# Kernel tuning notes

Measured on AMD Instinct MI355X. Metric: run time of the kernel, lower is better.

## Reference

```python
import jax, jax.numpy as jnp
import numpy as np

N_NODES = 50000
N_EDGES = 800000
D = 128
N_GRAPHS = 64
N_CLASSES = 10


def setup_inputs() -> dict:
    key = jax.random.key(0)
    ks = jax.random.split(key, 10)
    x = jax.random.normal(ks[0], (N_NODES, D), dtype=jnp.float32)
    edge_index = jax.random.randint(ks[1], (2, N_EDGES), 0, N_NODES, dtype=jnp.int64)
    batch = jnp.sort(jax.random.randint(ks[2], (N_NODES,), 0, N_GRAPHS, dtype=jnp.int64))
    s = 1.0 / np.sqrt(D)
    W1a = jax.random.uniform(ks[3], (D, D), jnp.float32, -s, s)
    W1b = jax.random.uniform(ks[4], (D, D), jnp.float32, -s, s)
    W2a = jax.random.uniform(ks[5], (D, D), jnp.float32, -s, s)
    W2b = jax.random.uniform(ks[6], (D, D), jnp.float32, -s, s)
    Wfc = jax.random.uniform(ks[7], (D, N_CLASSES), jnp.float32, -s, s)
    return {
        "x": x, "edge_index": edge_index, "batch": batch,
        "W1a": W1a, "b1a": jnp.zeros((D,), jnp.float32),
        "W1b": W1b, "b1b": jnp.zeros((D,), jnp.float32),
        "W2a": W2a, "b2a": jnp.zeros((D,), jnp.float32),
        "W2b": W2b, "b2b": jnp.zeros((D,), jnp.float32),
        "Wfc": Wfc, "bfc": jnp.zeros((N_CLASSES,), jnp.float32),
    }


def _gin_conv(x, src, dst, Wa, ba, Wb, bb):
    # sum aggregation of neighbor messages x[src] into dst (eps = 0)
    agg = jax.ops.segment_sum(x[src], dst, num_segments=N_NODES)
    h = x + agg  # (1 + eps) * x + sum_{j->i} x_j
    h = jax.nn.relu(h @ Wa + ba)
    h = jax.nn.relu(h @ Wb + bb)
    return h


def reference(x, edge_index, batch, W1a, b1a, W1b, b1b, W2a, b2a, W2b, b2b, Wfc, bfc):
    src, dst = edge_index[0], edge_index[1]
    h = _gin_conv(x, src, dst, W1a, b1a, W1b, b1b)
    h = _gin_conv(h, src, dst, W2a, b2a, W2b, b2b)
    # global mean pool over graphs
    sums = jax.ops.segment_sum(h, batch, num_segments=N_GRAPHS)
    counts = jax.ops.segment_sum(jnp.ones((h.shape[0], 1), h.dtype), batch, num_segments=N_GRAPHS)
    pooled = sums / jnp.maximum(counts, 1.0)
    logits = pooled @ Wfc + bfc
    return jax.nn.sigmoid(logits)
```

## Files before the change

### kernel.cpp

```cpp
#include <hip/hip_runtime.h>

#define NN 50000
#define NE 800000
#define DF 128
#define NG 64
#define NC 10
#define NBK 98
#define PART_CHUNK 4096
#define PART_GRID 196
#define ACAP 12288
#define FINE_CAP 12288
#define RT 136

typedef short bf16x8 __attribute__((ext_vector_type(8)));
typedef float f32x4  __attribute__((ext_vector_type(4)));

__device__ __forceinline__ void atomAddF(float* p, float v) {
  __hip_atomic_fetch_add(p, v, __ATOMIC_RELAXED, __HIP_MEMORY_SCOPE_AGENT);
}
__device__ __forceinline__ float b2f(unsigned short u) {
  union { unsigned int i; float f; } v; v.i = (unsigned int)u << 16; return v.f;
}
__device__ __forceinline__ unsigned int f2b(float f) {
  unsigned int i = __float_as_uint(f);
  return (i + 0x7fffu + ((i >> 16) & 1u)) >> 16;
}

__global__ __launch_bounds__(256) void k_cast(const float* __restrict__ x,
                                              unsigned short* __restrict__ xb)
{
  const int i = blockIdx.x * 256 + threadIdx.x;
  if (i * 4 >= NN * DF) return;
  const float4 v = reinterpret_cast<const float4*>(x)[i];
  uint2 o;
  o.x = f2b(v.x) | (f2b(v.y) << 16);
  o.y = f2b(v.z) | (f2b(v.w) << 16);
  reinterpret_cast<uint2*>(xb)[i] = o;
}

__global__ __launch_bounds__(256) void k_prepw(const float* __restrict__ W0,
                                               const float* __restrict__ W1,
                                               const float* __restrict__ W2,
                                               const float* __restrict__ W3,
                                               unsigned short* __restrict__ Wt)
{
  const int o = blockIdx.x * 256 + threadIdx.x;
  if (o >= 4 * 2048) return;
  const int mat = o >> 11;
  const float* W = (mat == 0) ? W0 : (mat == 1) ? W1 : (mat == 2) ? W2 : W3;
  const int rem = o & 2047;
  const int n  = rem >> 4;
  const int k0 = (rem & 15) * 8;
  unsigned int u[8];
#pragma unroll
  for (int j = 0; j < 8; ++j) u[j] = f2b(W[(size_t)(k0 + j) * DF + n]);
  uint4 p;
  p.x = u[0] | (u[1] << 16);
  p.y = u[2] | (u[3] << 16);
  p.z = u[4] | (u[5] << 16);
  p.w = u[6] | (u[7] << 16);
  *reinterpret_cast<uint4*>(Wt + (size_t)mat * DF * DF + (size_t)n * DF + k0) = p;
}

__global__ __launch_bounds__(256) void k_part(const int* __restrict__ src,
                                              const int* __restrict__ dst,
                                              int* __restrict__ cnt_b,
                                              unsigned int* __restrict__ arena)
{
  __shared__ unsigned int stage[PART_CHUNK];
  __shared__ int lhist[128], lcnt[128], lcur[128], gbase[128];
  const int tid = threadIdx.x;
  const int e0  = blockIdx.x * PART_CHUNK;
  const int nE  = min(PART_CHUNK, NE - e0);

  for (int i = tid; i < 128; i += 256) lhist[i] = 0;
  __syncthreads();

  unsigned int pk[16];
  int bk[16];
#pragma unroll
  for (int i = 0; i < 16; ++i) {
    const int e = e0 + i * 256 + tid;
    if (e < NE) {
      const int d = dst[e];
      const int s = src[e];
      const int b = d >> 9;
      bk[i] = b;
      pk[i] = ((unsigned int)b << 25) | ((unsigned int)(d & 511) << 16) | (unsigned int)s;
      atomicAdd(&lhist[b], 1);
    } else {
      bk[i] = -1;
    }
  }
  __syncthreads();
  for (int i = tid; i < 128; i += 256) lcnt[i] = lhist[i];
  __syncthreads();
  for (int off = 1; off < 128; off <<= 1) {
    int v = 0;
    if (tid < 128 && tid >= off) v = lhist[tid - off];
    __syncthreads();
    if (tid < 128) lhist[tid] += v;
    __syncthreads();
  }
  if (tid < 128) lcur[tid] = lhist[tid] - lcnt[tid];
  __syncthreads();
#pragma unroll
  for (int i = 0; i < 16; ++i) {
    if (bk[i] >= 0) {
      const int pos = atomicAdd(&lcur[bk[i]], 1);
      stage[pos] = pk[i];
    }
  }
  __syncthreads();
  if (tid < NBK) {
    const int c = lcnt[tid];
    if (c > 0) gbase[tid] = atomicAdd(&cnt_b[tid], c);
  }
  __syncthreads();
  for (int idx = tid; idx < nE; idx += 256) {
    const unsigned int p = stage[idx];
    const int b = (int)(p >> 25);
    const int loff = lhist[b] - lcnt[b];
    arena[(size_t)b * ACAP + gbase[b] + (idx - loff)] = p;
  }
}

__global__ __launch_bounds__(128) void k_bscan(const int* __restrict__ cnt_b,
                                               int* __restrict__ base_b,
                                               int* __restrict__ rs)
{
  __shared__ int sm[128];
  const int t = threadIdx.x;
  const int v = (t < NBK) ? cnt_b[t] : 0;
  sm[t] = v;
  __syncthreads();
  for (int off = 1; off < 128; off <<= 1) {
    int u = (t >= off) ? sm[t - off] : 0;
    __syncthreads();
    sm[t] += u;
    __syncthreads();
  }
  base_b[t] = sm[t] - v;
  if (t == NBK - 1) rs[NN] = sm[t];
}

__global__ __launch_bounds__(256) void k_fine(const unsigned int* __restrict__ arena,
                                              const int* __restrict__ cnt_b,
                                              const int* __restrict__ base_b,
                                              int* __restrict__ rs,
                                              unsigned short* __restrict__ es)
{
  __shared__ unsigned short les[FINE_CAP];
  __shared__ int bins[4096];
  __shared__ int partials[256];
  const int tid   = threadIdx.x;
  const int b     = blockIdx.x;
  const int cnt   = cnt_b[b];
  const int wbase = base_b[b];
  const int nbase = b << 9;
  const int nwin  = min(512, NN - nbase);
  const unsigned int* ap = arena + (size_t)b * ACAP;

  for (int i = tid; i < 4096; i += 256) bins[i] = 0;
  __syncthreads();
  for (int idx = tid; idx < cnt; idx += 256) {
    const unsigned int p = ap[idx];
    const int key = (int)(((p >> 16) & 511) << 3) | (int)((p & 0xffffu) >> 13);
    atomicAdd(&bins[key], 1);
  }
  __syncthreads();
  const int b16 = tid * 16;
  int sum = 0;
#pragma unroll
  for (int k = 0; k < 16; ++k) sum += bins[b16 + k];
  partials[tid] = sum;
  __syncthreads();
  for (int off = 1; off < 256; off <<= 1) {
    int u = (tid >= off) ? partials[tid - off] : 0;
    __syncthreads();
    partials[tid] += u;
    __syncthreads();
  }
  int run = partials[tid] - sum;
#pragma unroll
  for (int k = 0; k < 16; ++k) {
    const int v = bins[b16 + k];
    bins[b16 + k] = run;
    run += v;
  }
  __syncthreads();
  for (int i = tid; i < nwin; i += 256) rs[nbase + i] = wbase + bins[i << 3];
  __syncthreads();
  if (cnt <= FINE_CAP) {
    for (int idx = tid; idx < cnt; idx += 256) {
      const unsigned int p = ap[idx];
      const int key = (int)(((p >> 16) & 511) << 3) | (int)((p & 0xffffu) >> 13);
      const int pos = atomicAdd(&bins[key], 1);
      les[pos] = (unsigned short)(p & 0xffffu);
    }
    __syncthreads();
    for (int i = tid; i < cnt; i += 256) es[wbase + i] = les[i];
  } else {
    for (int idx = tid; idx < cnt; idx += 256) {
      const unsigned int p = ap[idx];
      const int key = (int)(((p >> 16) & 511) << 3) | (int)((p & 0xffffu) >> 13);
      const int pos = atomicAdd(&bins[key], 1);
      es[wbase + pos] = (unsigned short)(p & 0xffffu);
    }
  }
}

__global__ __launch_bounds__(256) void k_gather(const unsigned short* __restrict__ feat,
                                                unsigned short* __restrict__ outp,
                                                const int* __restrict__ rs,
                                                const unsigned short* __restrict__ es)
{
  const int wid  = (blockIdx.x * 256 + threadIdx.x) >> 6;
  const int lane = threadIdx.x & 63;
  if (wid >= NN) return;
  const int beg = rs[wid];
  const int end = rs[wid + 1];
  const int off = lane * 2;

  const unsigned int self = *reinterpret_cast<const unsigned int*>(feat + (size_t)wid * DF + off);
  float ax = b2f(self & 0xffff), ay = b2f(self >> 16);
  int j = beg;
  while (j < end && (j & 3)) {
    const int s = es[j];
    const unsigned int u = *reinterpret_cast<const unsigned int*>(feat + (size_t)s * DF + off);
    ax += b2f(u & 0xffff);
    ay += b2f(u >> 16);
    ++j;
  }
  for (; j + 3 < end; j += 4) {
    const uint2 e4 = *reinterpret_cast<const uint2*>(es + j);
    const int s0 = (int)(e4.x & 0xffffu), s1 = (int)(e4.x >> 16);
    const int s2 = (int)(e4.y & 0xffffu), s3 = (int)(e4.y >> 16);
    const unsigned int u0 = *reinterpret_cast<const unsigned int*>(feat + (size_t)s0 * DF + off);
    const unsigned int u1 = *reinterpret_cast<const unsigned int*>(feat + (size_t)s1 * DF + off);
    const unsigned int u2 = *reinterpret_cast<const unsigned int*>(feat + (size_t)s2 * DF + off);
    const unsigned int u3 = *reinterpret_cast<const unsigned int*>(feat + (size_t)s3 * DF + off);
    ax += b2f(u0 & 0xffff) + b2f(u1 & 0xffff) + b2f(u2 & 0xffff) + b2f(u3 & 0xffff);
    ay += b2f(u0 >> 16)    + b2f(u1 >> 16)    + b2f(u2 >> 16)    + b2f(u3 >> 16);
  }
  for (; j < end; ++j) {
    const int s = es[j];
    const unsigned int u = *reinterpret_cast<const unsigned int*>(feat + (size_t)s * DF + off);
    ax += b2f(u & 0xffff);
    ay += b2f(u >> 16);
  }
  const unsigned int o = f2b(ax) | (f2b(ay) << 16);
  *reinterpret_cast<unsigned int*>(outp + (size_t)wid * DF + off) = o;
}

__global__ __launch_bounds__(256) void k_gemm2(const unsigned short* __restrict__ Ab,
                                               const unsigned short* __restrict__ Wta,
                                               const float* __restrict__ ba,
                                               const unsigned short* __restrict__ Wtb,
                                               const float* __restrict__ bb,
                                               unsigned short* __restrict__ outb, int M)
{
  __shared__ unsigned short WbL[128 * 128];
  __shared__ unsigned short hL[4][16 * RT];
  const int tid  = threadIdx.x;
  const int lane = tid & 63;
  const int w    = tid >> 6;
  const int col  = lane & 15;
  const int kq   = lane >> 4;

  for (int i = tid; i < 2048; i += 256) {
    const int n = i >> 4, kb = i & 15;
    const int kbp = (kb + n) & 15;
    *reinterpret_cast<uint4*>(&WbL[n * 128 + kbp * 8]) =
        *reinterpret_cast<const uint4*>(&Wtb[(size_t)n * 128 + kb * 8]);
  }

  bf16x8 wfa[8][4];
#pragma unroll
  for (int nf = 0; nf < 8; ++nf)
#pragma unroll
    for (int s = 0; s < 4; ++s)
      wfa[nf][s] = *reinterpret_cast<const bf16x8*>(
          Wta + (size_t)(nf * 16 + col) * DF + s * 32 + kq * 8);

  __syncthreads();

  unsigned short* hw = &hL[w][0];
  const int rbase = blockIdx.x * 256;

  int m = rbase + w * 16 + col;
  int mld = (m < M) ? m : (M - 1);
  bf16x8 bc[4];
#pragma unroll
  for (int s = 0; s < 4; ++s)
    bc[s] = *reinterpret_cast<const bf16x8*>(Ab + (size_t)mld * DF + s * 32 + kq * 8);

#pragma unroll
  for (int t = 0; t < 4; ++t) {
    bf16x8 bn[4];
    if (t < 3) {
      const int m2 = rbase + (t + 1) * 64 + w * 16 + col;
      const int mld2 = (m2 < M) ? m2 : (M - 1);
#pragma unroll
      for (int s = 0; s < 4; ++s)
        bn[s] = *reinterpret_cast<const bf16x8*>(Ab + (size_t)mld2 * DF + s * 32 + kq * 8);
    }
    f32x4 acc[8];
#pragma unroll
    for (int nf = 0; nf < 8; ++nf) acc[nf] = (f32x4){0.f, 0.f, 0.f, 0.f};
#pragma unroll
    for (int s = 0; s < 4; ++s)
#pragma unroll
      for (int nf = 0; nf < 8; ++nf)
        acc[nf] = __builtin_amdgcn_mfma_f32_16x16x32_bf16(wfa[nf][s], bc[s], acc[nf], 0, 0, 0);
#pragma unroll
    for (int nf = 0; nf < 8; ++nf) {
      const float4 bv = *reinterpret_cast<const float4*>(ba + nf * 16 + kq * 4);
      uint2 pk;
      pk.x = f2b(fmaxf(acc[nf][0] + bv.x, 0.f)) | (f2b(fmaxf(acc[nf][1] + bv.y, 0.f)) << 16);
      pk.y = f2b(fmaxf(acc[nf][2] + bv.z, 0.f)) | (f2b(fmaxf(acc[nf][3] + bv.w, 0.f)) << 16);
      *reinterpret_cast<uint2*>(&hw[col * RT + nf * 16 + kq * 4]) = pk;
    }
    asm volatile("s_waitcnt lgkmcnt(0)" ::: "memory");
    __builtin_amdgcn_sched_barrier(0);
    f32x4 acc2[8];
#pragma unroll
    for (int nf = 0; nf < 8; ++nf) acc2[nf] = (f32x4){0.f, 0.f, 0.f, 0.f};
#pragma unroll
    for (int s = 0; s < 4; ++s) {
      const bf16x8 hb = *reinterpret_cast<const bf16x8*>(&hw[col * RT + s * 32 + kq * 8]);
#pragma unroll
      for (int nf = 0; nf < 8; ++nf) {
        const int kbp = (s * 4 + kq + col) & 15;
        const bf16x8 wb = *reinterpret_cast<const bf16x8*>(&WbL[(nf * 16 + col) * 128 + kbp * 8]);
        acc2[nf] = __builtin_amdgcn_mfma_f32_16x16x32_bf16(wb, hb, acc2[nf], 0, 0, 0);
      }
    }
    if (m < M) {
#pragma unroll
      for (int nf = 0; nf < 8; ++nf) {
        const float4 bv = *reinterpret_cast<const float4*>(bb + nf * 16 + kq * 4);
        ushort4 p;
        p.x = (unsigned short)f2b(fmaxf(acc2[nf][0] + bv.x, 0.f));
        p.y = (unsigned short)f2b(fmaxf(acc2[nf][1] + bv.y, 0.f));
        p.z = (unsigned short)f2b(fmaxf(acc2[nf][2] + bv.z, 0.f));
        p.w = (unsigned short)f2b(fmaxf(acc2[nf][3] + bv.w, 0.f));
        *reinterpret_cast<ushort4*>(outb + (size_t)m * DF + nf * 16 + kq * 4) = p;
      }
    }
#pragma unroll
    for (int s = 0; s < 4; ++s) bc[s] = bn[s];
    m = rbase + (t + 1) * 64 + w * 16 + col;
    mld = (m < M) ? m : (M - 1);
  }
}

__global__ __launch_bounds__(256) void k_pool(const unsigned short* __restrict__ h,
                                              const int* __restrict__ batch,
                                              float* __restrict__ sums,
                                              int* __restrict__ cnts)
{
  const int wv   = (blockIdx.x * 256 + threadIdx.x) >> 6;
  const int lane = threadIdx.x & 63;
  const int n0 = wv * 32;
  if (n0 >= NN) return;
  const int n1 = min(n0 + 32, NN);
  const int off = lane * 2;

  const int gfirst = batch[n0];
  const int glast  = batch[n1 - 1];
  float ax = 0.f, ay = 0.f;

  if (gfirst == glast) {
#pragma unroll 4
    for (int i = n0; i < n1; ++i) {
      const unsigned int u = *reinterpret_cast<const unsigned int*>(h + (size_t)i * DF + off);
      ax += b2f(u & 0xffff);
      ay += b2f(u >> 16);
    }
    atomAddF(&sums[gfirst * DF + off],     ax);
    atomAddF(&sums[gfirst * DF + off + 1], ay);
    if (lane == 0) atomicAdd(&cnts[gfirst], n1 - n0);
  } else {
    int g = gfirst, cnt = 0;
    for (int i = n0; i < n1; ++i) {
      const int gi = batch[i];
      if (gi != g) {
        atomAddF(&sums[g * DF + off],     ax);
        atomAddF(&sums[g * DF + off + 1], ay);
        if (lane == 0) atomicAdd(&cnts[g], cnt);
        ax = 0.f; ay = 0.f; cnt = 0; g = gi;
      }
      const unsigned int u = *reinterpret_cast<const unsigned int*>(h + (size_t)i * DF + off);
      ax += b2f(u & 0xffff);
      ay += b2f(u >> 16);
      ++cnt;
    }
    atomAddF(&sums[g * DF + off],     ax);
    atomAddF(&sums[g * DF + off + 1], ay);
    if (lane == 0) atomicAdd(&cnts[g], cnt);
  }
}

__global__ __launch_bounds__(256) void k_head(const float* __restrict__ sums,
                                              const int* __restrict__ cnts,
                                              const float* __restrict__ Wfc,
                                              const float* __restrict__ bfc,
                                              float* __restrict__ out)
{
  for (int o = threadIdx.x; o < NG * NC; o += 256) {
    const int g = o / NC, c = o % NC;
    const float inv = 1.f / fmaxf((float)cnts[g], 1.f);
    float z = bfc[c];
    for (int k = 0; k < DF; ++k)
      z = fmaf(sums[g * DF + k] * inv, Wfc[k * NC + c], z);
    out[o] = 1.f / (1.f + expf(-z));
  }
}

extern "C" void kernel_launch(void* const* d_in, const int* in_sizes, int n_in,
                              void* d_out, int out_size, void* d_ws, size_t ws_size,
                              hipStream_t stream)
{
  const float* x   = (const float*)d_in[0];
  const int*   ei  = (const int*)d_in[1];
  const int* batch = (const int*)d_in[2];
  const float* W1a = (const float*)d_in[3];
  const float* b1a = (const float*)d_in[4];
  const float* W1b = (const float*)d_in[5];
  const float* b1b = (const float*)d_in[6];
  const float* W2a = (const float*)d_in[7];
  const float* b2a = (const float*)d_in[8];
  const float* W2b = (const float*)d_in[9];
  const float* b2b = (const float*)d_in[10];
  const float* Wfc = (const float*)d_in[11];
  const float* bfc = (const float*)d_in[12];
  float* out = (float*)d_out;

  const int* src = ei;
  const int* dst = ei + NE;

  unsigned short* xb = (unsigned short*)d_ws;
  unsigned short* A  = xb + (size_t)NN * DF;
  unsigned short* H  = A + (size_t)NN * DF;
  unsigned short* Wt = H + (size_t)NN * DF;
  float* sums  = (float*)(Wt + (size_t)4 * DF * DF);
  int*   cnts  = (int*)(sums + NG * DF);
  int*   cnt_b = cnts + 64;
  int*   base_b= cnt_b + 128;
  int*   rs    = base_b + 128;
  unsigned short* es = (unsigned short*)(rs + (NN + 4));
  unsigned int* arena = (unsigned int*)(es + NE);

  unsigned short* Wt1a = Wt;
  unsigned short* Wt1b = Wt + DF * DF;
  unsigned short* Wt2a = Wt + 2 * DF * DF;
  unsigned short* Wt2b = Wt + 3 * DF * DF;

  const int gemm_grid   = (NN + 255) / 256;
  const int gather_grid = (NN * 64 + 255) / 256;
  const int pool_grid   = ((NN + 31) / 32 + 3) / 4;

  k_cast<<<(NN * DF / 4 + 255) / 256, 256, 0, stream>>>(x, xb);
  k_prepw<<<32, 256, 0, stream>>>(W1a, W1b, W2a, W2b, Wt);
  hipMemsetAsync(sums, 0, (size_t)(NG * DF + 64 + 128) * sizeof(float), stream);
  k_part<<<PART_GRID, 256, 0, stream>>>(src, dst, cnt_b, arena);
  k_bscan<<<1, 128, 0, stream>>>(cnt_b, base_b, rs);
  k_fine<<<NBK, 256, 0, stream>>>(arena, cnt_b, base_b, rs, es);

  k_gather<<<gather_grid, 256, 0, stream>>>(xb, A, rs, es);
  k_gemm2<<<gemm_grid, 256, 0, stream>>>(A, Wt1a, b1a, Wt1b, b1b, A, NN);

  k_gather<<<gather_grid, 256, 0, stream>>>(A, H, rs, es);
  k_gemm2<<<gemm_grid, 256, 0, stream>>>(H, Wt2a, b2a, Wt2b, b2b, H, NN);

  k_pool<<<pool_grid, 256, 0, stream>>>(H, batch, sums, cnts);
  k_head<<<1, 256, 0, stream>>>(sums, cnts, Wfc, bfc, out);
}
```

Baseline: 205.0 us.

## Reblock weights k-major and run fused MLP GEMM with 512-thread blocks

Changes the prepared weight layout so each (k-block, n) 8-element chunk is contiguous, which lets the second weight matrix be copied linearly into LDS and read without the skewed bank-swizzle. The fused two-layer GEMM now uses 512-thread blocks handling 128 rows each (one tile per wave) instead of 256-thread blocks that looped over 4 tiles with software prefetch. Biases are hoisted into registers. This trades the in-block prefetch pipelining and weight reuse across tiles for more parallelism and simpler code, and the new unswizzled LDS layout may bring bank conflicts.

New measurement: 191.6 us. 6.5% less time.

```diff
diff --git a/kernel.cpp b/kernel.cpp
--- a/kernel.cpp
+++ b/kernel.cpp
@@ -49,17 +49,17 @@
   const int mat = o >> 11;
   const float* W = (mat == 0) ? W0 : (mat == 1) ? W1 : (mat == 2) ? W2 : W3;
   const int rem = o & 2047;
-  const int n  = rem >> 4;
-  const int k0 = (rem & 15) * 8;
+  const int kb = rem >> 7;
+  const int n  = rem & 127;
   unsigned int u[8];
 #pragma unroll
-  for (int j = 0; j < 8; ++j) u[j] = f2b(W[(size_t)(k0 + j) * DF + n]);
+  for (int j = 0; j < 8; ++j) u[j] = f2b(W[(size_t)(kb * 8 + j) * DF + n]);
   uint4 p;
   p.x = u[0] | (u[1] << 16);
   p.y = u[2] | (u[3] << 16);
   p.z = u[4] | (u[5] << 16);
   p.w = u[6] | (u[7] << 16);
-  *reinterpret_cast<uint4*>(Wt + (size_t)mat * DF * DF + (size_t)n * DF + k0) = p;
+  *reinterpret_cast<uint4*>(Wt + (size_t)mat * DF * DF + (size_t)rem * 8) = p;
 }
 
 __global__ __launch_bounds__(256) void k_part(const int* __restrict__ src,
@@ -253,27 +253,24 @@
   *reinterpret_cast<unsigned int*>(outp + (size_t)wid * DF + off) = o;
 }
 
-__global__ __launch_bounds__(256) void k_gemm2(const unsigned short* __restrict__ Ab,
+__global__ __launch_bounds__(512) void k_gemm2(const unsigned short* __restrict__ Ab,
                                                const unsigned short* __restrict__ Wta,
                                                const float* __restrict__ ba,
                                                const unsigned short* __restrict__ Wtb,
                                                const float* __restrict__ bb,
                                                unsigned short* __restrict__ outb, int M)
 {
-  __shared__ unsigned short WbL[128 * 128];
-  __shared__ unsigned short hL[4][16 * RT];
+  __shared__ unsigned short WbL[2048 * 8];
+  __shared__ unsigned short hL[8][16 * RT];
   const int tid  = threadIdx.x;
   const int lane = tid & 63;
   const int w    = tid >> 6;
   const int col  = lane & 15;
   const int kq   = lane >> 4;
 
-  for (int i = tid; i < 2048; i += 256) {
-    const int n = i >> 4, kb = i & 15;
-    const int kbp = (kb + n) & 15;
-    *reinterpret_cast<uint4*>(&WbL[n * 128 + kbp * 8]) =
-        *reinterpret_cast<const uint4*>(&Wtb[(size_t)n * 128 + kb * 8]);
-  }
+  for (int i = tid; i < 2048; i += 512)
+    *reinterpret_cast<uint4*>(&WbL[i * 8]) =
+        *reinterpret_cast<const uint4*>(&Wtb[(size_t)i * 8]);
 
   bf16x8 wfa[8][4];
 #pragma unroll
@@ -281,77 +278,68 @@
 #pragma unroll
     for (int s = 0; s < 4; ++s)
       wfa[nf][s] = *reinterpret_cast<const bf16x8*>(
-          Wta + (size_t)(nf * 16 + col) * DF + s * 32 + kq * 8);
+          Wta + ((size_t)(s * 4 + kq) * 128 + nf * 16 + col) * 8);
+
+  float4 bva[8], bvb[8];
+#pragma unroll
+  for (int nf = 0; nf < 8; ++nf) {
+    bva[nf] = *reinterpret_cast<const float4*>(ba + nf * 16 + kq * 4);
+    bvb[nf] = *reinterpret_cast<const float4*>(bb + nf * 16 + kq * 4);
+  }
 
   __syncthreads();
 
   unsigned short* hw = &hL[w][0];
-  const int rbase = blockIdx.x * 256;
-
-  int m = rbase + w * 16 + col;
-  int mld = (m < M) ? m : (M - 1);
+  const int m   = blockIdx.x * 128 + w * 16 + col;
+  const int mld = (m < M) ? m : (M - 1);
+
   bf16x8 bc[4];
 #pragma unroll
   for (int s = 0; s < 4; ++s)
     bc[s] = *reinterpret_cast<const bf16x8*>(Ab + (size_t)mld * DF + s * 32 + kq * 8);
 
-#pragma unroll
-  for (int t = 0; t < 4; ++t) {
-    bf16x8 bn[4];
-    if (t < 3) {
-      const int m2 = rbase + (t + 1) * 64 + w * 16 + col;
-      const int mld2 = (m2 < M) ? m2 : (M - 1);
-#pragma unroll
-      for (int s = 0; s < 4; ++s)
-        bn[s] = *reinterpret_cast<const bf16x8*>(Ab + (size_t)mld2 * DF + s * 32 + kq * 8);
-    }
-    f32x4 acc[8];
-#pragma unroll
-    for (int nf = 0; nf < 8; ++nf) acc[nf] = (f32x4){0.f, 0.f, 0.f, 0.f};
-#pragma unroll
-    for (int s = 0; s < 4; ++s)
-#pragma unroll
-      for (int nf = 0; nf < 8; ++nf)
-        acc[nf] = __builtin_amdgcn_mfma_f32_16x16x32_bf16(wfa[nf][s], bc[s], acc[nf], 0, 0, 0);
+  f32x4 acc[8];
+#pragma unroll
+  for (int nf = 0; nf < 8; ++nf) acc[nf] = (f32x4){0.f, 0.f, 0.f, 0.f};
+#pragma unroll
+  for (int s = 0; s < 4; ++s)
+#pragma unroll
+    for (int nf = 0; nf < 8; ++nf)
+      acc[nf] = __builtin_amdgcn_mfma_f32_16x16x32_bf16(wfa[nf][s], bc[s], acc[nf], 0, 0, 0);
+
+#pragma unroll
+  for (int nf = 0; nf < 8; ++nf) {
+    uint2 pk;
+    pk.x = f2b(fmaxf(acc[nf][0] + bva[nf].x, 0.f)) | (f2b(fmaxf(acc[nf][1] + bva[nf].y, 0.f)) << 16);
+    pk.y = f2b(fmaxf(acc[nf][2] + bva[nf].z, 0.f)) | (f2b(fmaxf(acc[nf][3] + bva[nf].w, 0.f)) << 16);
+    *reinterpret_cast<uint2*>(&hw[col * RT + nf * 16 + kq * 4]) = pk;
+  }
+  asm volatile("s_waitcnt lgkmcnt(0)" ::: "memory");
+  __builtin_amdgcn_sched_barrier(0);
+
+  f32x4 acc2[8];
+#pragma unroll
+  for (int nf = 0; nf < 8; ++nf) acc2[nf] = (f32x4){0.f, 0.f, 0.f, 0.f};
+#pragma unroll
+  for (int s = 0; s < 4; ++s) {
+    const bf16x8 hb = *reinterpret_cast<const bf16x8*>(&hw[col * RT + s * 32 + kq * 8]);
 #pragma unroll
     for (int nf = 0; nf < 8; ++nf) {
-      const float4 bv = *reinterpret_cast<const float4*>(ba + nf * 16 + kq * 4);
-      uint2 pk;
-      pk.x = f2b(fmaxf(acc[nf][0] + bv.x, 0.f)) | (f2b(fmaxf(acc[nf][1] + bv.y, 0.f)) << 16);
-      pk.y = f2b(fmaxf(acc[nf][2] + bv.z, 0.f)) | (f2b(fmaxf(acc[nf][3] + bv.w, 0.f)) << 16);
-      *reinterpret_cast<uint2*>(&hw[col * RT + nf * 16 + kq * 4]) = pk;
-    }
-    asm volatile("s_waitcnt lgkmcnt(0)" ::: "memory");
-    __builtin_amdgcn_sched_barrier(0);
-    f32x4 acc2[8];
-#pragma unroll
-    for (int nf = 0; nf < 8; ++nf) acc2[nf] = (f32x4){0.f, 0.f, 0.f, 0.f};
-#pragma unroll
-    for (int s = 0; s < 4; ++s) {
-      const bf16x8 hb = *reinterpret_cast<const bf16x8*>(&hw[col * RT + s * 32 + kq * 8]);
-#pragma unroll
-      for (int nf = 0; nf < 8; ++nf) {
-        const int kbp = (s * 4 + kq + col) & 15;
-        const bf16x8 wb = *reinterpret_cast<const bf16x8*>(&WbL[(nf * 16 + col) * 128 + kbp * 8]);
-        acc2[nf] = __builtin_amdgcn_mfma_f32_16x16x32_bf16(wb, hb, acc2[nf], 0, 0, 0);
-      }
-    }
-    if (m < M) {
-#pragma unroll
-      for (int nf = 0; nf < 8; ++nf) {
-        const float4 bv = *reinterpret_cast<const float4*>(bb + nf * 16 + kq * 4);
-        ushort4 p;
-        p.x = (unsigned short)f2b(fmaxf(acc2[nf][0] + bv.x, 0.f));
-        p.y = (unsigned short)f2b(fmaxf(acc2[nf][1] + bv.y, 0.f));
-        p.z = (unsigned short)f2b(fmaxf(acc2[nf][2] + bv.z, 0.f));
-        p.w = (unsigned short)f2b(fmaxf(acc2[nf][3] + bv.w, 0.f));
-        *reinterpret_cast<ushort4*>(outb + (size_t)m * DF + nf * 16 + kq * 4) = p;
-      }
-    }
-#pragma unroll
-    for (int s = 0; s < 4; ++s) bc[s] = bn[s];
-    m = rbase + (t + 1) * 64 + w * 16 + col;
-    mld = (m < M) ? m : (M - 1);
+      const bf16x8 wb = *reinterpret_cast<const bf16x8*>(
+          &WbL[((s * 4 + kq) * 128 + nf * 16 + col) * 8]);
+      acc2[nf] = __builtin_amdgcn_mfma_f32_16x16x32_bf16(wb, hb, acc2[nf], 0, 0, 0);
+    }
+  }
+  if (m < M) {
+#pragma unroll
+    for (int nf = 0; nf < 8; ++nf) {
+      ushort4 p;
+      p.x = (unsigned short)f2b(fmaxf(acc2[nf][0] + bvb[nf].x, 0.f));
+      p.y = (unsigned short)f2b(fmaxf(acc2[nf][1] + bvb[nf].y, 0.f));
+      p.z = (unsigned short)f2b(fmaxf(acc2[nf][2] + bvb[nf].z, 0.f));
+      p.w = (unsigned short)f2b(fmaxf(acc2[nf][3] + bvb[nf].w, 0.f));
+      *reinterpret_cast<ushort4*>(outb + (size_t)m * DF + nf * 16 + kq * 4) = p;
+    }
   }
 }
 
@@ -457,7 +445,7 @@
   unsigned short* Wt2a = Wt + 2 * DF * DF;
   unsigned short* Wt2b = Wt + 3 * DF * DF;
 
-  const int gemm_grid   = (NN + 255) / 256;
+  const int gemm_grid   = (NN + 127) / 128;
   const int gather_grid = (NN * 64 + 255) / 256;
   const int pool_grid   = ((NN + 31) / 32 + 3) / 4;
 
@@ -469,10 +457,10 @@
   k_fine<<<NBK, 256, 0, stream>>>(arena, cnt_b, base_b, rs, es);
 
   k_gather<<<gather_grid, 256, 0, stream>>>(xb, A, rs, es);
-  k_gemm2<<<gemm_grid, 256, 0, stream>>>(A, Wt1a, b1a, Wt1b, b1b, A, NN);
+  k_gemm2<<<gemm_grid, 512, 0, stream>>>(A, Wt1a, b1a, Wt1b, b1b, A, NN);
 
   k_gather<<<gather_grid, 256, 0, stream>>>(A, H, rs, es);
-  k_gemm2<<<gemm_grid, 256, 0, stream>>>(H, Wt2a, b2a, Wt2b, b2b, H, NN);
+  k_gemm2<<<gemm_grid, 512, 0, stream>>>(H, Wt2a, b2a, Wt2b, b2b, H, NN);
 
   k_pool<<<pool_grid, 256, 0, stream>>>(H, batch, sums, cnts);
   k_head<<<1, 256, 0, stream>>>(sums, cnts, Wfc, bfc, out);
```
